# Kernel tuning notes

Hardware: AMD Instinct MI355X
Metric: run time of the kernel (lower is better)

Reference implementation:

```python
import jax, jax.numpy as jnp
import numpy as np

N, G, E, F, H = 65536, 32768, 600000, 128, 128

def _mlp(x, w1, b1, w2, b2):
    # Linear -> SiLU -> Linear
    return jax.nn.silu(x @ w1 + b1) @ w2 + b2

def setup_inputs() -> dict:
    key = jax.random.key(0)
    ks = jax.random.split(key, 24)
    def lin(k, din, dout):
        kw, kb = jax.random.split(k)
        s = 1.0 / np.sqrt(din)
        return (jax.random.uniform(kw, (din, dout), jnp.float32, -s, s),
                jax.random.uniform(kb, (dout,), jnp.float32, -s, s))
    nm_w1, nm_b1 = lin(ks[0], F, H)
    nm_w2, nm_b2 = lin(ks[1], H, H)
    em_w1, em_b1 = lin(ks[2], 6, H)
    em_w2, em_b2 = lin(ks[3], H, H)
    mm_w1, mm_b1 = lin(ks[4], 2 * H, H)
    mm_w2, mm_b2 = lin(ks[5], H, H)
    um_w1, um_b1 = lin(ks[6], H, H)
    um_w2, um_b2 = lin(ks[7], H, H)
    return {
        "node_features": jax.random.normal(ks[8], (N, F), jnp.float32),
        "node_pos": jax.random.uniform(ks[9], (N, 3), jnp.float32),
        "grid_pos": jax.random.uniform(ks[10], (G, 3), jnp.float32),
        "edge_index": jax.random.randint(ks[11], (2, E), 0, G, jnp.int64),
        "nm_w1": nm_w1, "nm_b1": nm_b1, "nm_w2": nm_w2, "nm_b2": nm_b2,
        "em_w1": em_w1, "em_b1": em_b1, "em_w2": em_w2, "em_b2": em_b2,
        "mm_w1": mm_w1, "mm_b1": mm_b1, "mm_w2": mm_w2, "mm_b2": mm_b2,
        "um_w1": um_w1, "um_b1": um_b1, "um_w2": um_w2, "um_b2": um_b2,
    }

def reference(node_features, node_pos, grid_pos, edge_index,
              nm_w1, nm_b1, nm_w2, nm_b2,
              em_w1, em_b1, em_w2, em_b2,
              mm_w1, mm_b1, mm_w2, mm_b2,
              um_w1, um_b1, um_w2, um_b2):
    src, tgt = edge_index[0], edge_index[1]
    # node_model on all points [N,H]
    nf = _mlp(node_features, nm_w1, nm_b1, nm_w2, nm_b2)
    # edge features from gathered positions [E,6] -> [E,H]
    edge_attr = jnp.concatenate([node_pos[src], grid_pos[tgt]], axis=-1)
    ef = _mlp(edge_attr, em_w1, em_b1, em_w2, em_b2)
    # messages [E,2H] -> [E,H]
    msg = _mlp(jnp.concatenate([nf[src], ef], axis=-1), mm_w1, mm_b1, mm_w2, mm_b2)
    # scatter-add mean aggregation to grid [G,H]
    counts = jax.ops.segment_sum(jnp.ones((msg.shape[0],), msg.dtype), tgt, num_segments=G)
    counts = jnp.maximum(counts, 1.0)[:, None]
    agg = jax.ops.segment_sum(msg, tgt, num_segments=G) / counts
    # update_model [G,H]
    return _mlp(agg, um_w1, um_b1, um_w2, um_b2)
```

## Files before the change

### kernel.cpp

```cpp
#include <hip/hip_runtime.h>

#define N_NODES 65536
#define G_GRID  32768
#define E_EDGES 600000
#define HD      128

typedef __attribute__((ext_vector_type(8))) short bf8;
typedef __attribute__((ext_vector_type(4))) float f32x4;

__device__ __forceinline__ short f2bf(float f){
  union { float f; unsigned u; } v; v.f = f;
  unsigned r = v.u + 0x7FFFu + ((v.u >> 16) & 1u);
  return (short)(r >> 16);
}
__device__ __forceinline__ float bf2f(short s){
  union { unsigned u; float f; } v; v.u = ((unsigned)(unsigned short)s) << 16; return v.f;
}

__device__ __forceinline__ bf8 load_pack8(const float* p, float scale){
  float4 u0 = *(const float4*)p;
  float4 u1 = *(const float4*)(p + 4);
  bf8 r;
  r[0]=f2bf(u0.x*scale); r[1]=f2bf(u0.y*scale); r[2]=f2bf(u0.z*scale); r[3]=f2bf(u0.w*scale);
  r[4]=f2bf(u1.x*scale); r[5]=f2bf(u1.y*scale); r[6]=f2bf(u1.z*scale); r[7]=f2bf(u1.w*scale);
  return r;
}

__global__ void prep_w_k(const float* __restrict__ nmw1, const float* __restrict__ nmw2,
                         const float* __restrict__ emw2, const float* __restrict__ mmw1,
                         const float* __restrict__ mmw2, const float* __restrict__ umw1,
                         const float* __restrict__ umw2, short* __restrict__ dst)
{
  int i = blockIdx.x*256 + threadIdx.x;
  const float* src; int local; bool k256 = false;
  if      (i < 16384){ src = nmw1; local = i; }
  else if (i < 32768){ src = nmw2; local = i - 16384; }
  else if (i < 49152){ src = emw2; local = i - 32768; }
  else if (i < 81920){ src = mmw1; local = i - 49152; k256 = true; }
  else if (i < 98304){ src = mmw2; local = i - 81920; }
  else if (i < 114688){ src = umw1; local = i - 98304; }
  else               { src = umw2; local = i - 114688; }
  int n, k;
  if (k256){ n = local >> 8; k = local & 255; }
  else     { n = local >> 7; k = local & 127; }
  dst[i] = f2bf(src[k*HD + n]);
}

__global__ void prep_combo2_k(const float* __restrict__ emw1, const float* __restrict__ eb1,
                              const float* __restrict__ emw2, const float* __restrict__ eb2,
                              const float* __restrict__ mmw1, const float* __restrict__ mb1,
                              short* __restrict__ wcombot, float* __restrict__ bcombo,
                              short* __restrict__ ew1x)
{
  if (blockIdx.x < 128){
    __shared__ float part[2][128];
    int k = blockIdx.x;
    int t = threadIdx.x, n = t & 127, half = t >> 7;
    float acc = 0.f;
    const float* er = emw2 + k*HD + half*64;
    #pragma unroll 8
    for (int j=0;j<64;j++) acc += er[j] * mmw1[(HD + half*64 + j)*HD + n];
    part[half][n] = acc;
    __syncthreads();
    if (half == 0) wcombot[n*HD + k] = f2bf(part[0][n] + part[1][n]);
  } else {
    int t = threadIdx.x;
    if (t < 128){
      int n = t;
      float acc = mb1[n];
      for (int j=0;j<HD;j++) acc += eb2[j] * mmw1[(HD + j)*HD + n];
      bcombo[n] = acc;
      short v[32];
      #pragma unroll
      for (int i=0;i<32;i++) v[i] = 0;
      #pragma unroll
      for (int i=0;i<6;i++){
        float wv = emw1[i*HD + n];
        short wh = f2bf(wv);
        short wl = f2bf(wv - bf2f(wh));
        v[i] = wh; v[6+i] = wh; v[12+i] = wl;
      }
      float bv = eb1[n];
      short bh = f2bf(bv);
      v[18] = bh; v[19] = f2bf(bv - bf2f(bh));
      #pragma unroll
      for (int i=0;i<32;i++) ew1x[n*32 + i] = v[i];
    }
  }
}

__global__ void node_mlp_k(const float* __restrict__ X,
                           const short* __restrict__ w1t, const float* __restrict__ b1,
                           const short* __restrict__ w2t, const float* __restrict__ b2,
                           short* __restrict__ nf)
{
  __shared__ short hid[64][136];
  const int t = threadIdx.x;
  const int wave = t >> 6, lane = t & 63, l15 = lane & 15, q = lane >> 4;
  const int rw = blockIdx.x*64 + wave*16;

  bf8 a[4];
  const float* xr = X + (size_t)(rw + l15)*HD;
  #pragma unroll
  for (int kt=0; kt<4; kt++) a[kt] = load_pack8(xr + kt*32 + q*8, 1.0f);

  #pragma unroll
  for (int ct=0; ct<8; ct++){
    f32x4 acc = {0.f,0.f,0.f,0.f};
    #pragma unroll
    for (int kt=0; kt<4; kt++){
      bf8 b = *(const bf8*)(w1t + (ct*16 + l15)*HD + kt*32 + q*8);
      acc = __builtin_amdgcn_mfma_f32_16x16x32_bf16(a[kt], b, acc, 0, 0, 0);
    }
    float bias = b1[ct*16 + l15];
    #pragma unroll
    for (int r=0;r<4;r++){
      float v = acc[r] + bias;
      v = v / (1.f + __expf(-v));
      hid[wave*16 + q*4 + r][ct*16 + l15] = f2bf(v);
    }
  }
  bf8 a2[4];
  #pragma unroll
  for (int kt=0;kt<4;kt++) a2[kt] = *(const bf8*)&hid[wave*16 + l15][kt*32 + q*8];
  #pragma unroll
  for (int ct=0; ct<8; ct++){
    f32x4 acc = {0.f,0.f,0.f,0.f};
    #pragma unroll
    for (int kt=0;kt<4;kt++){
      bf8 b = *(const bf8*)(w2t + (ct*16 + l15)*HD + kt*32 + q*8);
      acc = __builtin_amdgcn_mfma_f32_16x16x32_bf16(a2[kt], b, acc, 0, 0, 0);
    }
    float bias = b2[ct*16 + l15];
    #pragma unroll
    for (int r=0;r<4;r++)
      nf[(size_t)(rw + q*4 + r)*HD + ct*16 + l15] = f2bf(acc[r] + bias);
  }
}

__global__ void count_k(const int* __restrict__ eidx, int* __restrict__ counts){
  int e = blockIdx.x*256 + threadIdx.x;
  if (e < E_EDGES) atomicAdd(&counts[eidx[E_EDGES + e]], 1);
}

__global__ void scan_k(const int* __restrict__ counts, int* __restrict__ offs){
  __shared__ int part[1024];
  const int t = threadIdx.x;
  const int base = t*32;
  int loc[32];
  int s = 0;
  #pragma unroll
  for (int i=0;i<32;i++){ loc[i] = s; s += counts[base+i]; }
  part[t] = s;
  __syncthreads();
  for (int off=1; off<1024; off<<=1){
    int v = (t>=off) ? part[t-off] : 0;
    __syncthreads();
    part[t] += v;
    __syncthreads();
  }
  int pre = (t==0) ? 0 : part[t-1];
  #pragma unroll
  for (int i=0;i<32;i++) offs[base+i] = pre + loc[i];
  if (t==1023) offs[G_GRID] = pre + s;
}

__global__ void scatter_k(const int* __restrict__ eidx, const int* __restrict__ offs,
                          int* __restrict__ counts,
                          int* __restrict__ srcs_s, int* __restrict__ tgts_s){
  int e = blockIdx.x*256 + threadIdx.x;
  if (e < E_EDGES){
    int g = eidx[E_EDGES + e];
    int slot = offs[g] + atomicSub(&counts[g], 1) - 1;
    srcs_s[slot] = eidx[e];
    tgts_s[slot] = g;
  }
}

__device__ __forceinline__ bf8 build_af(const float p[6], int q){
  short ph[6], pl[6];
  #pragma unroll
  for (int i=0;i<6;i++){
    ph[i] = f2bf(p[i]);
    pl[i] = f2bf(p[i] - bf2f(ph[i]));
  }
  bf8 af = {0,0,0,0,0,0,0,0};
  if (q == 0){
    af[0]=ph[0]; af[1]=ph[1]; af[2]=ph[2]; af[3]=ph[3];
    af[4]=ph[4]; af[5]=ph[5]; af[6]=pl[0]; af[7]=pl[1];
  } else if (q == 1){
    af[0]=pl[2]; af[1]=pl[3]; af[2]=pl[4]; af[3]=pl[5];
    af[4]=ph[0]; af[5]=ph[1]; af[6]=ph[2]; af[7]=ph[3];
  } else if (q == 2){
    af[0]=ph[4]; af[1]=ph[5]; af[2]=(short)0x3F80; af[3]=(short)0x3F80;
  }
  return af;
}

__global__ void __launch_bounds__(256, 3)
edge_msg6_k(const int* __restrict__ srcs_s, const int* __restrict__ tgts_s,
            const float* __restrict__ npos, const float* __restrict__ gpos,
            const short* __restrict__ ew1x, const float* __restrict__ bcombo,
            const short* __restrict__ mw1t, const short* __restrict__ wcombot,
            const short* __restrict__ mw2t, const float* __restrict__ mb2,
            const short* __restrict__ nf, float* __restrict__ agg)
{
  __shared__ int tgtl[128];
  __shared__ short hm[128][136];

  const int t = threadIdx.x;
  const int e0 = blockIdx.x*128;
  const int w = t >> 6, lane = t & 63, l15 = lane & 15, q = lane >> 4;
  const int base = e0 + w*32;

  int i0 = base + l15;      if (i0 >= E_EDGES) i0 = E_EDGES - 1;
  int i1 = base + 16 + l15; if (i1 >= E_EDGES) i1 = E_EDGES - 1;
  int s0 = srcs_s[i0], s1 = srcs_s[i1];
  int g0 = tgts_s[i0], g1 = tgts_s[i1];

  bf8 an0[4], an1[4];
  {
    const short* n0p = nf + (size_t)s0*HD + q*8;
    const short* n1p = nf + (size_t)s1*HD + q*8;
    #pragma unroll
    for (int kt=0;kt<4;kt++){ an0[kt] = *(const bf8*)(n0p + kt*32); an1[kt] = *(const bf8*)(n1p + kt*32); }
  }
  float pA[6], pB[6];
  pA[0]=npos[s0*3+0]; pA[1]=npos[s0*3+1]; pA[2]=npos[s0*3+2];
  pA[3]=gpos[g0*3+0]; pA[4]=gpos[g0*3+1]; pA[5]=gpos[g0*3+2];
  pB[0]=npos[s1*3+0]; pB[1]=npos[s1*3+1]; pB[2]=npos[s1*3+2];
  pB[3]=gpos[g1*3+0]; pB[4]=gpos[g1*3+1]; pB[5]=gpos[g1*3+2];

  if (lane < 32){
    int idx = base + lane; if (idx >= E_EDGES) idx = E_EDGES - 1;
    tgtl[w*32 + lane] = tgts_s[idx];
  }

  bf8 af0 = build_af(pA, q);
  bf8 af1 = build_af(pB, q);
  #pragma unroll
  for (int ct=0; ct<8; ct++){
    bf8 bw = *(const bf8*)(ew1x + (ct*16 + l15)*32 + q*8);
    f32x4 h0 = {0.f,0.f,0.f,0.f}, h1 = {0.f,0.f,0.f,0.f};
    h0 = __builtin_amdgcn_mfma_f32_16x16x32_bf16(af0, bw, h0, 0,0,0);
    h1 = __builtin_amdgcn_mfma_f32_16x16x32_bf16(af1, bw, h1, 0,0,0);
    int col = ct*16 + l15;
    #pragma unroll
    for (int r=0;r<4;r++){
      float v0 = h0[r];
      v0 = v0 / (1.f + __expf(-v0));
      hm[w*32 + q*4 + r][col] = f2bf(v0);
      float v1 = h1[r];
      v1 = v1 / (1.f + __expf(-v1));
      hm[w*32 + 16 + q*4 + r][col] = f2bf(v1);
    }
  }

  bf8 ah0[4], ah1[4];
  #pragma unroll
  for (int kt=0;kt<4;kt++){
    ah0[kt] = *(const bf8*)&hm[w*32 + l15][kt*32 + q*8];
    ah1[kt] = *(const bf8*)&hm[w*32 + 16 + l15][kt*32 + q*8];
  }
  #pragma unroll
  for (int ct=0; ct<8; ct++){
    bf8 bw1[4], bwc[4];
    #pragma unroll
    for (int kt=0;kt<4;kt++){
      bw1[kt] = *(const bf8*)(mw1t + (ct*16 + l15)*256 + kt*32 + q*8);
      bwc[kt] = *(const bf8*)(wcombot + (ct*16 + l15)*HD + kt*32 + q*8);
    }
    f32x4 acc0 = {0.f,0.f,0.f,0.f}, acc1 = {0.f,0.f,0.f,0.f};
    #pragma unroll
    for (int kt=0;kt<4;kt++){
      acc0 = __builtin_amdgcn_mfma_f32_16x16x32_bf16(an0[kt], bw1[kt], acc0, 0,0,0);
      acc1 = __builtin_amdgcn_mfma_f32_16x16x32_bf16(an1[kt], bw1[kt], acc1, 0,0,0);
    }
    #pragma unroll
    for (int kt=0;kt<4;kt++){
      acc0 = __builtin_amdgcn_mfma_f32_16x16x32_bf16(ah0[kt], bwc[kt], acc0, 0,0,0);
      acc1 = __builtin_amdgcn_mfma_f32_16x16x32_bf16(ah1[kt], bwc[kt], acc1, 0,0,0);
    }
    float bias = bcombo[ct*16 + l15];
    int col = ct*16 + l15;
    #pragma unroll
    for (int r=0;r<4;r++){
      float v0 = acc0[r] + bias;
      v0 = v0 / (1.f + __expf(-v0));
      hm[w*32 + q*4 + r][col] = f2bf(v0);
      float v1 = acc1[r] + bias;
      v1 = v1 / (1.f + __expf(-v1));
      hm[w*32 + 16 + q*4 + r][col] = f2bf(v1);
    }
  }

  bf8 am0[4], am1[4];
  #pragma unroll
  for (int kt=0;kt<4;kt++){
    am0[kt] = *(const bf8*)&hm[w*32 + l15][kt*32 + q*8];
    am1[kt] = *(const bf8*)&hm[w*32 + 16 + l15][kt*32 + q*8];
  }

  float* msgf_w = (float*)&hm[w*32][0];
  int lim0 = E_EDGES - base;      if (lim0 > 16) lim0 = 16;
  int lim1 = E_EDGES - base - 16; if (lim1 > 16) lim1 = 16;
  int c2 = lane*2;
  int cur = -1; float sx = 0.f, sy = 0.f;

  #pragma unroll
  for (int ct=0; ct<8; ct++){
    f32x4 acc = {0.f,0.f,0.f,0.f};
    #pragma unroll
    for (int kt=0;kt<4;kt++){
      bf8 b = *(const bf8*)(mw2t + (ct*16 + l15)*HD + kt*32 + q*8);
      acc = __builtin_amdgcn_mfma_f32_16x16x32_bf16(am0[kt], b, acc, 0,0,0);
    }
    float bias = mb2[ct*16 + l15];
    int col = ct*16 + l15;
    #pragma unroll
    for (int r=0;r<4;r++) msgf_w[(q*4 + r)*132 + col] = acc[r] + bias;
  }
  if (lim0 > 0){
    cur = tgtl[w*32];
    for (int r=0; r<lim0; r++){
      int tg = tgtl[w*32 + r];
      float2 v = *(const float2*)&msgf_w[r*132 + c2];
      if (tg != cur){
        atomicAdd(&agg[(size_t)cur*HD + c2], sx);
        atomicAdd(&agg[(size_t)cur*HD + c2 + 1], sy);
        cur = tg; sx = v.x; sy = v.y;
      } else { sx += v.x; sy += v.y; }
    }
  }

  if (lim1 > 0){
    #pragma unroll
    for (int ct=0; ct<8; ct++){
      f32x4 acc = {0.f,0.f,0.f,0.f};
      #pragma unroll
      for (int kt=0;kt<4;kt++){
        bf8 b = *(const bf8*)(mw2t + (ct*16 + l15)*HD + kt*32 + q*8);
        acc = __builtin_amdgcn_mfma_f32_16x16x32_bf16(am1[kt], b, acc, 0,0,0);
      }
      float bias = mb2[ct*16 + l15];
      int col = ct*16 + l15;
      #pragma unroll
      for (int r=0;r<4;r++) msgf_w[(q*4 + r)*132 + col] = acc[r] + bias;
    }
    for (int r=0; r<lim1; r++){
      int tg = tgtl[w*32 + 16 + r];
      float2 v = *(const float2*)&msgf_w[r*132 + c2];
      if (tg != cur){
        atomicAdd(&agg[(size_t)cur*HD + c2], sx);
        atomicAdd(&agg[(size_t)cur*HD + c2 + 1], sy);
        cur = tg; sx = v.x; sy = v.y;
      } else { sx += v.x; sy += v.y; }
    }
  }
  if (cur >= 0){
    atomicAdd(&agg[(size_t)cur*HD + c2], sx);
    atomicAdd(&agg[(size_t)cur*HD + c2 + 1], sy);
  }
}

__global__ void update_mlp2_k(const float* __restrict__ agg, const int* __restrict__ offs,
                              const short* __restrict__ w1t, const float* __restrict__ b1,
                              const short* __restrict__ w2t, const float* __restrict__ b2,
                              float* __restrict__ out)
{
  __shared__ short hid[64][136];
  const int t = threadIdx.x;
  const int wave = t >> 6, lane = t & 63, l15 = lane & 15, q = lane >> 4;
  const int rw = blockIdx.x*64 + wave*16;

  int row = rw + l15;
  float c = (float)(offs[row+1] - offs[row]);
  float rcp = 1.0f / fmaxf(c, 1.0f);
  bf8 a[4];
  const float* ar = agg + (size_t)row*HD;
  #pragma unroll
  for (int kt=0; kt<4; kt++) a[kt] = load_pack8(ar + kt*32 + q*8, rcp);

  #pragma unroll
  for (int ct=0; ct<8; ct++){
    f32x4 acc = {0.f,0.f,0.f,0.f};
    #pragma unroll
    for (int kt=0; kt<4; kt++){
      bf8 b = *(const bf8*)(w1t + (ct*16 + l15)*HD + kt*32 + q*8);
      acc = __builtin_amdgcn_mfma_f32_16x16x32_bf16(a[kt], b, acc, 0, 0, 0);
    }
    float bias = b1[ct*16 + l15];
    #pragma unroll
    for (int r=0;r<4;r++){
      float v = acc[r] + bias;
      v = v / (1.f + __expf(-v));
      hid[wave*16 + q*4 + r][ct*16 + l15] = f2bf(v);
    }
  }
  bf8 a2[4];
  #pragma unroll
  for (int kt=0;kt<4;kt++) a2[kt] = *(const bf8*)&hid[wave*16 + l15][kt*32 + q*8];
  #pragma unroll
  for (int ct=0; ct<8; ct++){
    f32x4 acc = {0.f,0.f,0.f,0.f};
    #pragma unroll
    for (int kt=0;kt<4;kt++){
      bf8 b = *(const bf8*)(w2t + (ct*16 + l15)*HD + kt*32 + q*8);
      acc = __builtin_amdgcn_mfma_f32_16x16x32_bf16(a2[kt], b, acc, 0, 0, 0);
    }
    float bias = b2[ct*16 + l15];
    #pragma unroll
    for (int r=0;r<4;r++)
      out[(size_t)(rw + q*4 + r)*HD + ct*16 + l15] = acc[r] + bias;
  }
}

extern "C" void kernel_launch(void* const* d_in, const int* in_sizes, int n_in,
                              void* d_out, int out_size, void* d_ws, size_t ws_size,
                              hipStream_t stream)
{
  const float* node_features = (const float*)d_in[0];
  const float* node_pos      = (const float*)d_in[1];
  const float* grid_pos      = (const float*)d_in[2];
  const int*   edge_index    = (const int*)d_in[3];
  const float* nm_w1 = (const float*)d_in[4];
  const float* nm_b1 = (const float*)d_in[5];
  const float* nm_w2 = (const float*)d_in[6];
  const float* nm_b2 = (const float*)d_in[7];
  const float* em_w1 = (const float*)d_in[8];
  const float* em_b1 = (const float*)d_in[9];
  const float* em_w2 = (const float*)d_in[10];
  const float* em_b2 = (const float*)d_in[11];
  const float* mm_w1 = (const float*)d_in[12];
  const float* mm_b1 = (const float*)d_in[13];
  const float* mm_w2 = (const float*)d_in[14];
  const float* mm_b2 = (const float*)d_in[15];
  const float* um_w1 = (const float*)d_in[16];
  const float* um_b1 = (const float*)d_in[17];
  const float* um_w2 = (const float*)d_in[18];
  const float* um_b2 = (const float*)d_in[19];
  float* out = (float*)d_out;

  char* ws = (char*)d_ws;
  short* nf     = (short*)ws;
  int*   counts = (int*)  (ws + 16777216ull);
  int*   offs   = (int*)  (ws + 16908288ull);
  short* wts    = (short*)(ws + 17039424ull);
  short* wcombot= (short*)(ws + 17301568ull);
  float* bcombo = (float*)(ws + 17334336ull);
  short* ew1x   = (short*)(ws + 17334848ull);
  int*   srcs_s = (int*)  (ws + 17343040ull);
  int*   tgts_s = (int*)  (ws + 19743040ull);

  short* nmw1t = wts;
  short* nmw2t = wts + 16384;
  short* mmw1t = wts + 49152;
  short* mmw2t = wts + 81920;
  short* umw1t = wts + 98304;
  short* umw2t = wts + 114688;

  float* agg = out;

  (void)hipMemsetAsync(counts, 0, 131072, stream);
  (void)hipMemsetAsync(out, 0, (size_t)G_GRID*HD*4, stream);

  prep_w_k<<<512, 256, 0, stream>>>(nm_w1, nm_w2, em_w2, mm_w1, mm_w2, um_w1, um_w2, wts);
  prep_combo2_k<<<129, 256, 0, stream>>>(em_w1, em_b1, em_w2, em_b2, mm_w1, mm_b1,
                                         wcombot, bcombo, ew1x);
  node_mlp_k<<<G_GRID/64, 256, 0, stream>>>(node_features, nmw1t, nm_b1, nmw2t, nm_b2, nf);
  count_k<<<(E_EDGES+255)/256, 256, 0, stream>>>(edge_index, counts);
  scan_k<<<1, 1024, 0, stream>>>(counts, offs);
  scatter_k<<<(E_EDGES+255)/256, 256, 0, stream>>>(edge_index, offs, counts, srcs_s, tgts_s);
  edge_msg6_k<<<(E_EDGES + 127)/128, 256, 0, stream>>>(srcs_s, tgts_s, node_pos, grid_pos,
      ew1x, bcombo, mmw1t, wcombot, mmw2t, mm_b2, nf, agg);
  update_mlp2_k<<<G_GRID/64, 256, 0, stream>>>(agg, offs, umw1t, um_b1, umw2t, um_b2, out);
}
```

Baseline: 543.4 us.

## Merge setup kernels and pre-gather edge positions into sorted pos buffer

Folds weight prep, combo-weight prep and the edge count atomics into one setup kernel launch. The scatter kernel now also gathers node and grid positions into a padded 8-float-per-edge buffer in sorted order. The edge message kernel then reads them with two vector loads instead of six scattered scalar gathers per edge. This adds about 19MB of extra writes and reads and more scattered work inside scatter_k, in exchange for fewer launches and coalesced position loads in the hot kernel.

```diff
diff --git a/kernel.cpp b/kernel.cpp
--- a/kernel.cpp
+++ b/kernel.cpp
@@ -26,35 +26,35 @@
   return r;
 }
 
-__global__ void prep_w_k(const float* __restrict__ nmw1, const float* __restrict__ nmw2,
-                         const float* __restrict__ emw2, const float* __restrict__ mmw1,
-                         const float* __restrict__ mmw2, const float* __restrict__ umw1,
-                         const float* __restrict__ umw2, short* __restrict__ dst)
+__global__ void setup_k(const float* __restrict__ nmw1, const float* __restrict__ nmw2,
+                        const float* __restrict__ mmw1, const float* __restrict__ mmw2,
+                        const float* __restrict__ umw1, const float* __restrict__ umw2,
+                        const float* __restrict__ emw1, const float* __restrict__ eb1,
+                        const float* __restrict__ emw2, const float* __restrict__ eb2,
+                        const float* __restrict__ mb1,
+                        const int* __restrict__ eidx,
+                        short* __restrict__ wts, short* __restrict__ wcombot,
+                        float* __restrict__ bcombo, short* __restrict__ ew1x,
+                        int* __restrict__ counts)
 {
-  int i = blockIdx.x*256 + threadIdx.x;
-  const float* src; int local; bool k256 = false;
-  if      (i < 16384){ src = nmw1; local = i; }
-  else if (i < 32768){ src = nmw2; local = i - 16384; }
-  else if (i < 49152){ src = emw2; local = i - 32768; }
-  else if (i < 81920){ src = mmw1; local = i - 49152; k256 = true; }
-  else if (i < 98304){ src = mmw2; local = i - 81920; }
-  else if (i < 114688){ src = umw1; local = i - 98304; }
-  else               { src = umw2; local = i - 114688; }
-  int n, k;
-  if (k256){ n = local >> 8; k = local & 255; }
-  else     { n = local >> 7; k = local & 127; }
-  dst[i] = f2bf(src[k*HD + n]);
-}
-
-__global__ void prep_combo2_k(const float* __restrict__ emw1, const float* __restrict__ eb1,
-                              const float* __restrict__ emw2, const float* __restrict__ eb2,
-                              const float* __restrict__ mmw1, const float* __restrict__ mb1,
-                              short* __restrict__ wcombot, float* __restrict__ bcombo,
-                              short* __restrict__ ew1x)
-{
-  if (blockIdx.x < 128){
+  const int b = blockIdx.x;
+  if (b < 512){
+    int i = b*256 + threadIdx.x;
+    const float* src; int local; bool k256 = false;
+    if      (i < 16384){ src = nmw1; local = i; }
+    else if (i < 32768){ src = nmw2; local = i - 16384; }
+    else if (i < 49152){ src = emw2; local = i - 32768; }
+    else if (i < 81920){ src = mmw1; local = i - 49152; k256 = true; }
+    else if (i < 98304){ src = mmw2; local = i - 81920; }
+    else if (i < 114688){ src = umw1; local = i - 98304; }
+    else               { src = umw2; local = i - 114688; }
+    int n, k;
+    if (k256){ n = local >> 8; k = local & 255; }
+    else     { n = local >> 7; k = local & 127; }
+    wts[i] = f2bf(src[k*HD + n]);
+  } else if (b < 640){
     __shared__ float part[2][128];
-    int k = blockIdx.x;
+    int k = b - 512;
     int t = threadIdx.x, n = t & 127, half = t >> 7;
     float acc = 0.f;
     const float* er = emw2 + k*HD + half*64;
@@ -63,7 +63,7 @@
     part[half][n] = acc;
     __syncthreads();
     if (half == 0) wcombot[n*HD + k] = f2bf(part[0][n] + part[1][n]);
-  } else {
+  } else if (b == 640){
     int t = threadIdx.x;
     if (t < 128){
       int n = t;
@@ -86,6 +86,9 @@
       #pragma unroll
       for (int i=0;i<32;i++) ew1x[n*32 + i] = v[i];
     }
+  } else {
+    int e = (b - 641)*256 + threadIdx.x;
+    if (e < E_EDGES) atomicAdd(&counts[eidx[E_EDGES + e]], 1);
   }
 }
 
@@ -138,11 +141,6 @@
   }
 }
 
-__global__ void count_k(const int* __restrict__ eidx, int* __restrict__ counts){
-  int e = blockIdx.x*256 + threadIdx.x;
-  if (e < E_EDGES) atomicAdd(&counts[eidx[E_EDGES + e]], 1);
-}
-
 __global__ void scan_k(const int* __restrict__ counts, int* __restrict__ offs){
   __shared__ int part[1024];
   const int t = threadIdx.x;
@@ -167,13 +165,20 @@
 
 __global__ void scatter_k(const int* __restrict__ eidx, const int* __restrict__ offs,
                           int* __restrict__ counts,
-                          int* __restrict__ srcs_s, int* __restrict__ tgts_s){
+                          int* __restrict__ srcs_s, int* __restrict__ tgts_s,
+                          const float* __restrict__ npos, const float* __restrict__ gpos,
+                          float* __restrict__ pos6){
   int e = blockIdx.x*256 + threadIdx.x;
   if (e < E_EDGES){
+    int s = eidx[e];
     int g = eidx[E_EDGES + e];
     int slot = offs[g] + atomicSub(&counts[g], 1) - 1;
-    srcs_s[slot] = eidx[e];
+    srcs_s[slot] = s;
     tgts_s[slot] = g;
+    float* pd = pos6 + (size_t)slot*8;
+    pd[0]=npos[s*3+0]; pd[1]=npos[s*3+1]; pd[2]=npos[s*3+2];
+    pd[3]=gpos[g*3+0]; pd[4]=gpos[g*3+1]; pd[5]=gpos[g*3+2];
+    pd[6]=0.f; pd[7]=0.f;
   }
 }
 
@@ -198,8 +203,8 @@
 }
 
 __global__ void __launch_bounds__(256, 3)
-edge_msg6_k(const int* __restrict__ srcs_s, const int* __restrict__ tgts_s,
-            const float* __restrict__ npos, const float* __restrict__ gpos,
+edge_msg7_k(const int* __restrict__ srcs_s, const int* __restrict__ tgts_s,
+            const float* __restrict__ pos6,
             const short* __restrict__ ew1x, const float* __restrict__ bcombo,
             const short* __restrict__ mw1t, const short* __restrict__ wcombot,
             const short* __restrict__ mw2t, const float* __restrict__ mb2,
@@ -216,7 +221,6 @@
   int i0 = base + l15;      if (i0 >= E_EDGES) i0 = E_EDGES - 1;
   int i1 = base + 16 + l15; if (i1 >= E_EDGES) i1 = E_EDGES - 1;
   int s0 = srcs_s[i0], s1 = srcs_s[i1];
-  int g0 = tgts_s[i0], g1 = tgts_s[i1];
 
   bf8 an0[4], an1[4];
   {
@@ -226,10 +230,16 @@
     for (int kt=0;kt<4;kt++){ an0[kt] = *(const bf8*)(n0p + kt*32); an1[kt] = *(const bf8*)(n1p + kt*32); }
   }
   float pA[6], pB[6];
-  pA[0]=npos[s0*3+0]; pA[1]=npos[s0*3+1]; pA[2]=npos[s0*3+2];
-  pA[3]=gpos[g0*3+0]; pA[4]=gpos[g0*3+1]; pA[5]=gpos[g0*3+2];
-  pB[0]=npos[s1*3+0]; pB[1]=npos[s1*3+1]; pB[2]=npos[s1*3+2];
-  pB[3]=gpos[g1*3+0]; pB[4]=gpos[g1*3+1]; pB[5]=gpos[g1*3+2];
+  {
+    const float* pp = pos6 + (size_t)i0*8;
+    f32x4 u0 = *(const f32x4*)pp;
+    f32x4 u1 = *(const f32x4*)(pp + 4);
+    pA[0]=u0[0]; pA[1]=u0[1]; pA[2]=u0[2]; pA[3]=u0[3]; pA[4]=u1[0]; pA[5]=u1[1];
+    const float* pq = pos6 + (size_t)i1*8;
+    f32x4 v0 = *(const f32x4*)pq;
+    f32x4 v1 = *(const f32x4*)(pq + 4);
+    pB[0]=v0[0]; pB[1]=v0[1]; pB[2]=v0[2]; pB[3]=v0[3]; pB[4]=v1[0]; pB[5]=v1[1];
+  }
 
   if (lane < 32){
     int idx = base + lane; if (idx >= E_EDGES) idx = E_EDGES - 1;
@@ -451,6 +461,7 @@
   short* ew1x   = (short*)(ws + 17334848ull);
   int*   srcs_s = (int*)  (ws + 17343040ull);
   int*   tgts_s = (int*)  (ws + 19743040ull);
+  float* pos6   = (float*)(ws + 22143040ull);
 
   short* nmw1t = wts;
   short* nmw2t = wts + 16384;
@@ -464,14 +475,14 @@
   (void)hipMemsetAsync(counts, 0, 131072, stream);
   (void)hipMemsetAsync(out, 0, (size_t)G_GRID*HD*4, stream);
 
-  prep_w_k<<<512, 256, 0, stream>>>(nm_w1, nm_w2, em_w2, mm_w1, mm_w2, um_w1, um_w2, wts);
-  prep_combo2_k<<<129, 256, 0, stream>>>(em_w1, em_b1, em_w2, em_b2, mm_w1, mm_b1,
-                                         wcombot, bcombo, ew1x);
+  const int count_blocks = (E_EDGES + 255)/256;
+  setup_k<<<641 + count_blocks, 256, 0, stream>>>(nm_w1, nm_w2, mm_w1, mm_w2, um_w1, um_w2,
+      em_w1, em_b1, em_w2, em_b2, mm_b1, edge_index, wts, wcombot, bcombo, ew1x, counts);
   node_mlp_k<<<G_GRID/64, 256, 0, stream>>>(node_features, nmw1t, nm_b1, nmw2t, nm_b2, nf);
-  count_k<<<(E_EDGES+255)/256, 256, 0, stream>>>(edge_index, counts);
   scan_k<<<1, 1024, 0, stream>>>(counts, offs);
-  scatter_k<<<(E_EDGES+255)/256, 256, 0, stream>>>(edge_index, offs, counts, srcs_s, tgts_s);
-  edge_msg6_k<<<(E_EDGES + 127)/128, 256, 0, stream>>>(srcs_s, tgts_s, node_pos, grid_pos,
+  scatter_k<<<count_blocks, 256, 0, stream>>>(edge_index, offs, counts, srcs_s, tgts_s,
+      node_pos, grid_pos, pos6);
+  edge_msg7_k<<<(E_EDGES + 127)/128, 256, 0, stream>>>(srcs_s, tgts_s, pos6,
       ew1x, bcombo, mmw1t, wcombot, mmw2t, mm_b2, nf, agg);
   update_mlp2_k<<<G_GRID/64, 256, 0, stream>>>(agg, offs, umw1t, um_b1, umw2t, um_b2, out);
 }
```

Result: faster. 528.4 us (-2.8%).
